# Optimization experiments

Measured on AMD Instinct MI355X. Metric: run time of the kernel, lower is better.

Reference implementation:

```python
import jax, jax.numpy as jnp
import numpy as np

NUM_HEADS = 8
NUM_LEVELS = 4
NUM_POINTS = 4
EMBED = 256
OFFSET_SCALE = 1.0
SPATIAL = [(96, 96), (48, 48), (24, 24), (12, 12)]  # (H_l, W_l) per level


def _grid_sample_bilinear(fmap, grid):
    """fmap: (N, C, H, W); grid: (N, Q, K, 2) with (x, y) in [-1, 1].
    Bilinear, align_corners=True. Locations are pre-clamped to [-1,1] so
    index clipping reproduces torch zeros-padding behavior exactly."""
    N, C, H, W = fmap.shape
    x = (grid[..., 0] + 1.0) * 0.5 * (W - 1)
    y = (grid[..., 1] + 1.0) * 0.5 * (H - 1)
    x0 = jnp.floor(x)
    y0 = jnp.floor(y)
    wx = (x - x0)[:, None]  # (N,1,Q,K)
    wy = (y - y0)[:, None]
    x0i = jnp.clip(x0.astype(jnp.int32), 0, W - 1)
    x1i = jnp.clip(x0i + 1, 0, W - 1)
    y0i = jnp.clip(y0.astype(jnp.int32), 0, H - 1)
    y1i = jnp.clip(y0i + 1, 0, H - 1)
    flat = fmap.reshape(N, C, H * W)
    Q, K = grid.shape[1], grid.shape[2]

    def g(yi, xi):
        idx = (yi * W + xi).reshape(N, 1, Q * K)
        return jnp.take_along_axis(flat, idx, axis=2).reshape(N, C, Q, K)

    return ((1 - wy) * ((1 - wx) * g(y0i, x0i) + wx * g(y0i, x1i))
            + wy * ((1 - wx) * g(y1i, x0i) + wx * g(y1i, x1i)))


def setup_inputs() -> dict:
    key = jax.random.key(0)
    ks = jax.random.split(key, 8)
    B, Q, E = 2, 12240, EMBED
    H, L, K = NUM_HEADS, NUM_LEVELS, NUM_POINTS
    Vlen = sum(h * w for h, w in SPATIAL)
    s = 0.02
    queries = jax.random.normal(ks[0], (B, Q, E), jnp.float32)
    ref_points = 2.0 * jax.random.uniform(ks[1], (B, Q, L, 2), jnp.float32) - 1.0
    value = jax.random.normal(ks[2], (B, Vlen, E), jnp.float32)
    Wv = jax.random.normal(ks[3], (E, E), jnp.float32) * s
    Woff = jax.random.normal(ks[4], (E, H * L * K * 2), jnp.float32) * s
    boff = jnp.zeros((H * L * K * 2,), jnp.float32)
    Wattn = jax.random.normal(ks[5], (E, H * L * K), jnp.float32) * s
    battn = jnp.zeros((H * L * K,), jnp.float32)
    Wout = jax.random.normal(ks[6], (E, E), jnp.float32) * s
    vss = jnp.array(SPATIAL, dtype=jnp.int32)
    return {"queries": queries, "ref_points": ref_points, "value": value,
            "Wv": Wv, "Woff": Woff, "boff": boff, "Wattn": Wattn,
            "battn": battn, "Wout": Wout, "value_spatial_shapes": vss}


def _forward(queries, ref_points, value, Wv, Woff, boff, Wattn, battn, Wout, spatial):
    B, Q, E = queries.shape
    H, L, K = NUM_HEADS, NUM_LEVELS, NUM_POINTS
    hd = E // H
    Vlen = value.shape[1]
    # offsets MLP (tanh) and attention weights
    offsets = OFFSET_SCALE * jnp.tanh(queries @ Woff + boff)
    offsets = offsets.reshape(B, Q, H, L, K, 2)
    attn = jax.nn.softmax((queries @ Wattn + battn).reshape(B, Q, H, L * K), axis=-1)
    attn = attn.reshape(B, Q, H, L, K).transpose(0, 2, 3, 1, 4).reshape(B * H, L, Q, K)
    # value projection -> (B*H, head_dim, Vlen)
    v = (value @ Wv).reshape(B, Vlen, H, hd).transpose(0, 2, 3, 1).reshape(B * H, hd, Vlen)
    # sampling locations (B*H, L, Q, K, 2)
    locs = jnp.clip(ref_points[:, :, None, :, None, :] + offsets, -1.0, 1.0)
    locs = locs.transpose(0, 2, 3, 1, 4, 5).reshape(B * H, L, Q, K, 2)
    # per-level bilinear sample + weighted accumulate
    sizes = [h * w for h, w in spatial]
    starts = np.concatenate([[0], np.cumsum(sizes)])
    acc = jnp.zeros((B * H, hd, Q, K), jnp.float32)
    for lvl, (Hl, Wl) in enumerate(spatial):
        fmap = v[:, :, starts[lvl]:starts[lvl + 1]].reshape(B * H, hd, Hl, Wl)
        samp = _grid_sample_bilinear(fmap, locs[:, lvl])  # (B*H, hd, Q, K)
        acc = acc + samp * attn[:, lvl][:, None]
    out = acc.reshape(B, E, Q, K).transpose(0, 2, 1, 3).sum(axis=-1)  # (B, Q, E)
    return out @ Wout


def reference(queries, ref_points, value, Wv, Woff, boff, Wattn, battn, Wout, value_spatial_shapes):
    spatial = [tuple(int(x) for x in row) for row in np.asarray(value_spatial_shapes)]
    return _forward(queries, ref_points, value, Wv, Woff, boff, Wattn, battn, Wout, spatial)
```

## Files before the change

kernel.cpp:

```cpp
#include <hip/hip_runtime.h>
#include <math.h>

#define NB 2
#define NQ 12240
#define NH 8
#define NL 4
#define NK 4
#define VLEN 12240
#define M_TOT (NB * NQ)
#define MT (M_TOT / 16)

typedef __attribute__((ext_vector_type(4))) float f32x4;
typedef __attribute__((ext_vector_type(8))) short bf16x8;
typedef __attribute__((ext_vector_type(8))) unsigned short u16x8;

__device__ __forceinline__ ushort f2bf(float x) {
    union { float f; unsigned u; } v; v.f = x;
    unsigned r = v.u + 0x7fffu + ((v.u >> 16) & 1u);
    return (ushort)(r >> 16);
}
__device__ __forceinline__ float bf2f(ushort h) {
    union { unsigned u; float f; } v; v.u = ((unsigned)h) << 16; return v.f;
}

__global__ __launch_bounds__(256) void preconv_B(
    const float* __restrict__ Woff, const float* __restrict__ Wattn,
    const float* __restrict__ Wv,   const float* __restrict__ Wout,
    ushort* __restrict__ Bp)
{
    const int gg = blockIdx.x * 256 + threadIdx.x;
    const float* W; ushort* H; ushort* L; int N, tl;
    if (gg < 8192)       { W = Woff;  H = Bp + 0;      L = Bp + 98304;  N = 256; tl = gg; }
    else if (gg < 12288) { W = Wattn; H = Bp + 65536;  L = Bp + 163840; N = 128; tl = gg - 8192; }
    else if (gg < 20480) { W = Wv;    H = Bp + 196608; L = Bp + 262144; N = 256; tl = gg - 12288; }
    else                 { W = Wout;  H = Bp + 327680; L = Bp + 393216; N = 256; tl = gg - 20480; }
    const int l  = tl & 63;
    const int kt = (tl >> 6) & 7;
    const int nt = tl >> 9;
    const int colb = nt * 16 + (l & 15);
    const int krow = kt * 32 + ((l >> 4) << 3);
    ushort h8[8], l8[8];
    #pragma unroll
    for (int j = 0; j < 8; ++j) {
        float x = W[(size_t)(krow + j) * N + colb];
        h8[j] = f2bf(x);
        l8[j] = f2bf(x - bf2f(h8[j]));
    }
    *(ushort4*)(H + (size_t)tl * 8)     = *(ushort4*)&h8[0];
    *(ushort4*)(H + (size_t)tl * 8 + 4) = *(ushort4*)&h8[4];
    *(ushort4*)(L + (size_t)tl * 8)     = *(ushort4*)&l8[0];
    *(ushort4*)(L + (size_t)tl * 8 + 4) = *(ushort4*)&l8[4];
}

__global__ __launch_bounds__(384) void gemm_qv(
    const float* __restrict__ Qf, const float* __restrict__ Vf,
    const ushort* __restrict__ Bp,
    const float* __restrict__ bias, const float* __restrict__ bias2,
    const float* __restrict__ ref,
    float* __restrict__ locC, float* __restrict__ attC,
    ushort* __restrict__ vC)
{
    const int wave = threadIdx.x >> 6;
    const int lane = threadIdx.x & 63;
    const bool isV = (blockIdx.x >= MT);
    const int mt   = isV ? (blockIdx.x - MT) : blockIdx.x;
    if (isV && wave >= 4) return;
    const int nt0 = wave * 4;
    const int lr = lane & 15, r0g = (lane >> 4) * 4;
    const int rowb = mt * 16 + r0g;

    const float* Af = (isV ? Vf : Qf) + (size_t)(mt * 16 + lr) * 256 + ((lane >> 4) << 3);

    f32x4 acc[4] = {};

    if (!isV) {
        const ushort* BH = Bp;
        const ushort* BL = Bp + 98304;
        #pragma unroll
        for (int kt = 0; kt < 8; ++kt) {
            float4 a0 = *(const float4*)(Af + kt * 32);
            float4 a1 = *(const float4*)(Af + kt * 32 + 4);
            union { bf16x8 v; ushort u[8]; } ah, al;
            #pragma unroll
            for (int j = 0; j < 4; ++j) {
                float x = (&a0.x)[j];
                ushort hv = f2bf(x);
                ah.u[j] = hv; al.u[j] = f2bf(x - bf2f(hv));
            }
            #pragma unroll
            for (int j = 0; j < 4; ++j) {
                float x = (&a1.x)[j];
                ushort hv = f2bf(x);
                ah.u[4 + j] = hv; al.u[4 + j] = f2bf(x - bf2f(hv));
            }
            bf16x8 bh[4], bl[4];
            #pragma unroll
            for (int fn = 0; fn < 4; ++fn) {
                size_t off = (((size_t)(nt0 + fn) * 8 + kt) * 64 + lane) * 8;
                bh[fn] = *(const bf16x8*)(BH + off);
                bl[fn] = *(const bf16x8*)(BL + off);
            }
            #pragma unroll
            for (int fn = 0; fn < 4; ++fn) {
                acc[fn] = __builtin_amdgcn_mfma_f32_16x16x32_bf16(ah.v, bh[fn], acc[fn], 0, 0, 0);
                acc[fn] = __builtin_amdgcn_mfma_f32_16x16x32_bf16(ah.v, bl[fn], acc[fn], 0, 0, 0);
                acc[fn] = __builtin_amdgcn_mfma_f32_16x16x32_bf16(al.v, bh[fn], acc[fn], 0, 0, 0);
            }
        }
        if (wave < 4) {
            #pragma unroll
            for (int fn = 0; fn < 4; ++fn) {
                const int c  = wave * 64 + fn * 16 + lr;
                const int l  = (c >> 3) & 3;
                const int xy = c & 1;
                const float sc = 0.5f * (float)(96 >> l) - 0.5f;
                const float b = bias[c];
                #pragma unroll
                for (int r = 0; r < 4; ++r) {
                    const int row = rowb + r;
                    const float rp = ref[(size_t)row * 8 + l * 2 + xy];
                    const float t  = tanhf(acc[fn][r] + b);
                    const float lc = fminf(fmaxf(rp + t, -1.f), 1.f);
                    locC[(size_t)row * 256 + c] = (lc + 1.f) * sc;
                }
            }
        } else {
            #pragma unroll
            for (int fn = 0; fn < 4; ++fn) {
                const int hcol = (wave - 4) * 64 + fn * 16 + lr;
                const float b = bias2[hcol];
                #pragma unroll
                for (int r = 0; r < 4; ++r) {
                    float e = expf(acc[fn][r] + b);
                    float s = e;
                    s += __shfl_xor(s, 1);
                    s += __shfl_xor(s, 2);
                    s += __shfl_xor(s, 4);
                    s += __shfl_xor(s, 8);
                    attC[(size_t)(rowb + r) * 128 + hcol] = e / s;
                }
            }
        }
    } else {
        const ushort* BH = Bp + 196608;
        #pragma unroll
        for (int kt = 0; kt < 8; ++kt) {
            float4 a0 = *(const float4*)(Af + kt * 32);
            float4 a1 = *(const float4*)(Af + kt * 32 + 4);
            union { bf16x8 v; ushort u[8]; } ah;
            #pragma unroll
            for (int j = 0; j < 4; ++j) ah.u[j]     = f2bf((&a0.x)[j]);
            #pragma unroll
            for (int j = 0; j < 4; ++j) ah.u[4 + j] = f2bf((&a1.x)[j]);
            bf16x8 bh[4];
            #pragma unroll
            for (int fn = 0; fn < 4; ++fn) {
                size_t off = (((size_t)(nt0 + fn) * 8 + kt) * 64 + lane) * 8;
                bh[fn] = *(const bf16x8*)(BH + off);
            }
            #pragma unroll
            for (int fn = 0; fn < 4; ++fn)
                acc[fn] = __builtin_amdgcn_mfma_f32_16x16x32_bf16(ah.v, bh[fn], acc[fn], 0, 0, 0);
        }
        #pragma unroll
        for (int fn = 0; fn < 4; ++fn) {
            const int col = (nt0 + fn) * 16 + lr;
            #pragma unroll
            for (int r = 0; r < 4; ++r)
                vC[(size_t)(rowb + r) * 256 + col] = f2bf(acc[fn][r]);
        }
    }
}

__global__ __launch_bounds__(256) void sample_kernel(
    const ushort* __restrict__ v_bf,
    const float* __restrict__ locs,
    const float* __restrict__ attnw,
    ushort* __restrict__ AccH)
{
    __shared__ float sloc[64][36];
    __shared__ float satt[64][20];

    const int h   = blockIdx.x & 7;
    const int qc  = blockIdx.x >> 3;
    const int tid = threadIdx.x;

    #pragma unroll
    for (int i = 0; i < 2; ++i) {
        int idx = tid + i * 256;
        int row = idx >> 3;
        int c   = (idx & 7) * 4;
        int bqr = qc * 64 + row;
        float4 v = make_float4(0.f, 0.f, 0.f, 0.f);
        if (bqr < M_TOT) v = *(const float4*)(locs + (size_t)bqr * 256 + h * 32 + c);
        *(float4*)&sloc[row][c] = v;
    }
    {
        int row = tid >> 2;
        int c   = (tid & 3) * 4;
        int bqr = qc * 64 + row;
        float4 v = make_float4(0.f, 0.f, 0.f, 0.f);
        if (bqr < M_TOT) v = *(const float4*)(attnw + (size_t)bqr * 128 + h * 16 + c);
        *(float4*)&satt[row][c] = v;
    }
    __syncthreads();

    const int qi = tid >> 2;
    const int c8 = tid & 3;
    const int bq = qc * 64 + qi;
    const int b  = (bq >= NQ) ? 1 : 0;
    const ushort* vbase = v_bf + ((size_t)b * VLEN) * 256 + h * 32 + c8 * 8;

    float acc[8] = {};
    #pragma unroll
    for (int l = 0; l < NL; ++l) {
        const int Wl = 96 >> l;
        const int st = (l == 0) ? 0 : (l == 1) ? 9216 : (l == 2) ? 11520 : 12096;
        #pragma unroll
        for (int k = 0; k < NK; ++k) {
            float px = sloc[qi][(l * 4 + k) * 2 + 0];
            float py = sloc[qi][(l * 4 + k) * 2 + 1];
            float w  = satt[qi][l * 4 + k];
            float x0f = floorf(px), y0f = floorf(py);
            float wx = px - x0f, wy = py - y0f;
            int x0 = (int)x0f, y0 = (int)y0f;
            x0 = min(max(x0, 0), Wl - 1);
            y0 = min(max(y0, 0), Wl - 1);
            int x1 = min(x0 + 1, Wl - 1);
            int y1 = min(y0 + 1, Wl - 1);
            float w11 = w * wy * wx;
            float w10 = w * wy - w11;
            float w01 = w * wx - w11;
            float w00 = w - w01 - w10 - w11;
            const ushort* r0 = vbase + (size_t)(st + y0 * Wl) * 256;
            const ushort* r1 = vbase + (size_t)(st + y1 * Wl) * 256;
            u16x8 u00 = *(const u16x8*)(r0 + (size_t)x0 * 256);
            u16x8 u01 = *(const u16x8*)(r0 + (size_t)x1 * 256);
            u16x8 u10 = *(const u16x8*)(r1 + (size_t)x0 * 256);
            u16x8 u11 = *(const u16x8*)(r1 + (size_t)x1 * 256);
            #pragma unroll
            for (int j = 0; j < 8; ++j) {
                acc[j] += w00 * bf2f(u00[j]) + w01 * bf2f(u01[j])
                        + w10 * bf2f(u10[j]) + w11 * bf2f(u11[j]);
            }
        }
    }

    if (bq < M_TOT) {
        const int mt  = bq >> 4;
        const int lfr = (c8 << 4) | (bq & 15);
        const size_t base = (((size_t)mt * 8 + h) * 64 + lfr) * 8;
        u16x8 hh;
        #pragma unroll
        for (int j = 0; j < 8; ++j) hh[j] = f2bf(acc[j]);
        *(u16x8*)(AccH + base) = hh;
    }
}

__global__ __launch_bounds__(256) void gemm_out(
    const ushort* __restrict__ Ah,
    const ushort* __restrict__ Bh, const ushort* __restrict__ Bl,
    float* __restrict__ C)
{
    const int wave = threadIdx.x >> 6;
    const int lane = threadIdx.x & 63;
    const int mt   = blockIdx.x;
    const int nt0  = wave * 4;

    f32x4 acc[4] = {};
    const ushort* aH = Ah + ((size_t)mt * 8 * 64 + lane) * 8;

    #pragma unroll
    for (int kt = 0; kt < 8; ++kt) {
        bf16x8 ah = *(const bf16x8*)(aH + kt * 512);
        bf16x8 bh[4], bl[4];
        #pragma unroll
        for (int fn = 0; fn < 4; ++fn) {
            size_t off = (((size_t)(nt0 + fn) * 8 + kt) * 64 + lane) * 8;
            bh[fn] = *(const bf16x8*)(Bh + off);
            bl[fn] = *(const bf16x8*)(Bl + off);
        }
        #pragma unroll
        for (int fn = 0; fn < 4; ++fn) {
            acc[fn] = __builtin_amdgcn_mfma_f32_16x16x32_bf16(ah, bh[fn], acc[fn], 0, 0, 0);
            acc[fn] = __builtin_amdgcn_mfma_f32_16x16x32_bf16(ah, bl[fn], acc[fn], 0, 0, 0);
        }
    }

    const int lr = lane & 15, r0 = (lane >> 4) * 4;
    const int rowb = mt * 16 + r0;
    #pragma unroll
    for (int fn = 0; fn < 4; ++fn) {
        const int col = (nt0 + fn) * 16 + lr;
        #pragma unroll
        for (int r = 0; r < 4; ++r)
            C[(size_t)(rowb + r) * 256 + col] = acc[fn][r];
    }
}

extern "C" void kernel_launch(void* const* d_in, const int* in_sizes, int n_in,
                              void* d_out, int out_size, void* d_ws, size_t ws_size,
                              hipStream_t stream)
{
    const float* queries = (const float*)d_in[0];
    const float* refpts  = (const float*)d_in[1];
    const float* value   = (const float*)d_in[2];
    const float* Wv      = (const float*)d_in[3];
    const float* Woff    = (const float*)d_in[4];
    const float* boff    = (const float*)d_in[5];
    const float* Wattn   = (const float*)d_in[6];
    const float* battn   = (const float*)d_in[7];
    const float* Wout    = (const float*)d_in[8];
    float* out = (float*)d_out;

    char* ws = (char*)d_ws;
    float*  off_ws  = (float*)(ws);
    float*  attn_ws = (float*)(ws + 25067520);
    ushort* v_bf    = (ushort*)(ws + 37601280);
    ushort* AccH    = (ushort*)(ws + 50135040);
    ushort* Bp      = (ushort*)(ws + 87736320);

    preconv_B<<<112, 256, 0, stream>>>(Woff, Wattn, Wv, Wout, Bp);
    gemm_qv<<<3060, 384, 0, stream>>>(queries, value, Bp, boff, battn, refpts,
                                      off_ws, attn_ws, v_bf);
    sample_kernel<<<3064, 256, 0, stream>>>(v_bf, off_ws, attn_ws, AccH);
    gemm_out<<<1530, 256, 0, stream>>>(AccH, Bp + 327680, Bp + 393216, out);
}
```

Measured before the change: 231.1 us.

## Switch intermediates to fp16, drop Wout low split, and process two M-tiles per block

Replaces bf16 storage and MFMA with fp16 throughout: weight pre-splitting, value projection, sampled accumulator and output GEMM, with packed cvt_pkrtz conversions instead of manual bf16 rounding. The output GEMM no longer uses a hi/lo split of Wout, which halves its B loads and MFMAs. The QV and output GEMMs each handle two 16-row tiles per block so every B fragment is reused twice, which halves the grid sizes. The fp16 range and round-toward-zero conversions trade some accuracy and overflow headroom for cheaper conversion and fewer MFMAs.

```diff
diff --git a/kernel.cpp b/kernel.cpp
--- a/kernel.cpp
+++ b/kernel.cpp
@@ -11,172 +11,183 @@
 #define MT (M_TOT / 16)
 
 typedef __attribute__((ext_vector_type(4))) float f32x4;
-typedef __attribute__((ext_vector_type(8))) short bf16x8;
-typedef __attribute__((ext_vector_type(8))) unsigned short u16x8;
-
-__device__ __forceinline__ ushort f2bf(float x) {
-    union { float f; unsigned u; } v; v.f = x;
-    unsigned r = v.u + 0x7fffu + ((v.u >> 16) & 1u);
-    return (ushort)(r >> 16);
-}
-__device__ __forceinline__ float bf2f(ushort h) {
-    union { unsigned u; float f; } v; v.u = ((unsigned)h) << 16; return v.f;
-}
+typedef __fp16 f16;
+typedef __attribute__((ext_vector_type(8))) __fp16 f16x8;
+typedef __attribute__((ext_vector_type(2))) __fp16 f16x2;
+
+#define BP_FL 98304
+#define BP_WV 196608
+#define BP_WO 262144
 
 __global__ __launch_bounds__(256) void preconv_B(
     const float* __restrict__ Woff, const float* __restrict__ Wattn,
     const float* __restrict__ Wv,   const float* __restrict__ Wout,
-    ushort* __restrict__ Bp)
+    f16* __restrict__ Bp)
 {
     const int gg = blockIdx.x * 256 + threadIdx.x;
-    const float* W; ushort* H; ushort* L; int N, tl;
-    if (gg < 8192)       { W = Woff;  H = Bp + 0;      L = Bp + 98304;  N = 256; tl = gg; }
-    else if (gg < 12288) { W = Wattn; H = Bp + 65536;  L = Bp + 163840; N = 128; tl = gg - 8192; }
-    else if (gg < 20480) { W = Wv;    H = Bp + 196608; L = Bp + 262144; N = 256; tl = gg - 12288; }
-    else                 { W = Wout;  H = Bp + 327680; L = Bp + 393216; N = 256; tl = gg - 20480; }
+    const float* W; f16* H; f16* L; int N, tl; bool two;
+    if (gg < 8192)       { W = Woff;  H = Bp;           L = Bp + BP_FL;         N = 256; tl = gg;         two = true;  }
+    else if (gg < 12288) { W = Wattn; H = Bp + 65536;   L = Bp + BP_FL + 65536; N = 128; tl = gg - 8192;  two = true;  }
+    else if (gg < 20480) { W = Wv;    H = Bp + BP_WV;   L = nullptr;            N = 256; tl = gg - 12288; two = false; }
+    else                 { W = Wout;  H = Bp + BP_WO;   L = nullptr;            N = 256; tl = gg - 20480; two = false; }
     const int l  = tl & 63;
     const int kt = (tl >> 6) & 7;
     const int nt = tl >> 9;
     const int colb = nt * 16 + (l & 15);
     const int krow = kt * 32 + ((l >> 4) << 3);
-    ushort h8[8], l8[8];
+    union { f16 f[8]; ushort4 u[2]; } h8, l8;
     #pragma unroll
     for (int j = 0; j < 8; ++j) {
         float x = W[(size_t)(krow + j) * N + colb];
-        h8[j] = f2bf(x);
-        l8[j] = f2bf(x - bf2f(h8[j]));
-    }
-    *(ushort4*)(H + (size_t)tl * 8)     = *(ushort4*)&h8[0];
-    *(ushort4*)(H + (size_t)tl * 8 + 4) = *(ushort4*)&h8[4];
-    *(ushort4*)(L + (size_t)tl * 8)     = *(ushort4*)&l8[0];
-    *(ushort4*)(L + (size_t)tl * 8 + 4) = *(ushort4*)&l8[4];
-}
-
-__global__ __launch_bounds__(384) void gemm_qv(
+        f16 hv = (f16)x;
+        h8.f[j] = hv;
+        l8.f[j] = (f16)(x - (float)hv);
+    }
+    *(ushort4*)(H + (size_t)tl * 8)     = h8.u[0];
+    *(ushort4*)(H + (size_t)tl * 8 + 4) = h8.u[1];
+    if (two) {
+        *(ushort4*)(L + (size_t)tl * 8)     = l8.u[0];
+        *(ushort4*)(L + (size_t)tl * 8 + 4) = l8.u[1];
+    }
+}
+
+__global__ __launch_bounds__(384, 3) void gemm_qv(
     const float* __restrict__ Qf, const float* __restrict__ Vf,
-    const ushort* __restrict__ Bp,
+    const f16* __restrict__ Bp,
     const float* __restrict__ bias, const float* __restrict__ bias2,
     const float* __restrict__ ref,
     float* __restrict__ locC, float* __restrict__ attC,
-    ushort* __restrict__ vC)
+    f16* __restrict__ vC)
 {
     const int wave = threadIdx.x >> 6;
     const int lane = threadIdx.x & 63;
-    const bool isV = (blockIdx.x >= MT);
-    const int mt   = isV ? (blockIdx.x - MT) : blockIdx.x;
+    const bool isV = (blockIdx.x >= 765);
+    const int mt0  = (isV ? (blockIdx.x - 765) : blockIdx.x) * 2;
     if (isV && wave >= 4) return;
     const int nt0 = wave * 4;
     const int lr = lane & 15, r0g = (lane >> 4) * 4;
-    const int rowb = mt * 16 + r0g;
-
-    const float* Af = (isV ? Vf : Qf) + (size_t)(mt * 16 + lr) * 256 + ((lane >> 4) << 3);
-
-    f32x4 acc[4] = {};
+
+    const float* A0 = (isV ? Vf : Qf) + (size_t)(mt0 * 16 + lr) * 256 + ((lane >> 4) << 3);
+    const float* A1 = A0 + 16 * 256;
+
+    f32x4 acc[2][4] = {};
 
     if (!isV) {
-        const ushort* BH = Bp;
-        const ushort* BL = Bp + 98304;
+        const f16* BH = Bp;
+        const f16* BL = Bp + BP_FL;
         #pragma unroll
         for (int kt = 0; kt < 8; ++kt) {
-            float4 a0 = *(const float4*)(Af + kt * 32);
-            float4 a1 = *(const float4*)(Af + kt * 32 + 4);
-            union { bf16x8 v; ushort u[8]; } ah, al;
-            #pragma unroll
-            for (int j = 0; j < 4; ++j) {
-                float x = (&a0.x)[j];
-                ushort hv = f2bf(x);
-                ah.u[j] = hv; al.u[j] = f2bf(x - bf2f(hv));
-            }
-            #pragma unroll
-            for (int j = 0; j < 4; ++j) {
-                float x = (&a1.x)[j];
-                ushort hv = f2bf(x);
-                ah.u[4 + j] = hv; al.u[4 + j] = f2bf(x - bf2f(hv));
-            }
-            bf16x8 bh[4], bl[4];
+            f16x8 bh[4], bl[4];
             #pragma unroll
             for (int fn = 0; fn < 4; ++fn) {
                 size_t off = (((size_t)(nt0 + fn) * 8 + kt) * 64 + lane) * 8;
-                bh[fn] = *(const bf16x8*)(BH + off);
-                bl[fn] = *(const bf16x8*)(BL + off);
-            }
-            #pragma unroll
-            for (int fn = 0; fn < 4; ++fn) {
-                acc[fn] = __builtin_amdgcn_mfma_f32_16x16x32_bf16(ah.v, bh[fn], acc[fn], 0, 0, 0);
-                acc[fn] = __builtin_amdgcn_mfma_f32_16x16x32_bf16(ah.v, bl[fn], acc[fn], 0, 0, 0);
-                acc[fn] = __builtin_amdgcn_mfma_f32_16x16x32_bf16(al.v, bh[fn], acc[fn], 0, 0, 0);
-            }
-        }
-        if (wave < 4) {
-            #pragma unroll
-            for (int fn = 0; fn < 4; ++fn) {
-                const int c  = wave * 64 + fn * 16 + lr;
-                const int l  = (c >> 3) & 3;
-                const int xy = c & 1;
-                const float sc = 0.5f * (float)(96 >> l) - 0.5f;
-                const float b = bias[c];
-                #pragma unroll
-                for (int r = 0; r < 4; ++r) {
-                    const int row = rowb + r;
-                    const float rp = ref[(size_t)row * 8 + l * 2 + xy];
-                    const float t  = tanhf(acc[fn][r] + b);
-                    const float lc = fminf(fmaxf(rp + t, -1.f), 1.f);
-                    locC[(size_t)row * 256 + c] = (lc + 1.f) * sc;
+                bh[fn] = *(const f16x8*)(BH + off);
+                bl[fn] = *(const f16x8*)(BL + off);
+            }
+            #pragma unroll
+            for (int m = 0; m < 2; ++m) {
+                const float* Af = m ? A1 : A0;
+                float4 a0 = *(const float4*)(Af + kt * 32);
+                float4 a1 = *(const float4*)(Af + kt * 32 + 4);
+                union { f16x8 v; f16x2 h[4]; } ah, al;
+                ah.h[0] = __builtin_amdgcn_cvt_pkrtz(a0.x, a0.y);
+                ah.h[1] = __builtin_amdgcn_cvt_pkrtz(a0.z, a0.w);
+                ah.h[2] = __builtin_amdgcn_cvt_pkrtz(a1.x, a1.y);
+                ah.h[3] = __builtin_amdgcn_cvt_pkrtz(a1.z, a1.w);
+                al.h[0] = __builtin_amdgcn_cvt_pkrtz(a0.x - (float)ah.h[0][0], a0.y - (float)ah.h[0][1]);
+                al.h[1] = __builtin_amdgcn_cvt_pkrtz(a0.z - (float)ah.h[1][0], a0.w - (float)ah.h[1][1]);
+                al.h[2] = __builtin_amdgcn_cvt_pkrtz(a1.x - (float)ah.h[2][0], a1.y - (float)ah.h[2][1]);
+                al.h[3] = __builtin_amdgcn_cvt_pkrtz(a1.z - (float)ah.h[3][0], a1.w - (float)ah.h[3][1]);
+                #pragma unroll
+                for (int fn = 0; fn < 4; ++fn) {
+                    acc[m][fn] = __builtin_amdgcn_mfma_f32_16x16x32_f16(ah.v, bh[fn], acc[m][fn], 0, 0, 0);
+                    acc[m][fn] = __builtin_amdgcn_mfma_f32_16x16x32_f16(ah.v, bl[fn], acc[m][fn], 0, 0, 0);
+                    acc[m][fn] = __builtin_amdgcn_mfma_f32_16x16x32_f16(al.v, bh[fn], acc[m][fn], 0, 0, 0);
                 }
             }
-        } else {
-            #pragma unroll
-            for (int fn = 0; fn < 4; ++fn) {
-                const int hcol = (wave - 4) * 64 + fn * 16 + lr;
-                const float b = bias2[hcol];
-                #pragma unroll
-                for (int r = 0; r < 4; ++r) {
-                    float e = expf(acc[fn][r] + b);
-                    float s = e;
-                    s += __shfl_xor(s, 1);
-                    s += __shfl_xor(s, 2);
-                    s += __shfl_xor(s, 4);
-                    s += __shfl_xor(s, 8);
-                    attC[(size_t)(rowb + r) * 128 + hcol] = e / s;
+        }
+        #pragma unroll
+        for (int m = 0; m < 2; ++m) {
+            const int rowb = (mt0 + m) * 16 + r0g;
+            if (wave < 4) {
+                #pragma unroll
+                for (int fn = 0; fn < 4; ++fn) {
+                    const int c  = wave * 64 + fn * 16 + lr;
+                    const int l  = (c >> 3) & 3;
+                    const int xy = c & 1;
+                    const float sc = 0.5f * (float)(96 >> l) - 0.5f;
+                    const float b = bias[c];
+                    #pragma unroll
+                    for (int r = 0; r < 4; ++r) {
+                        const int row = rowb + r;
+                        const float rp = ref[(size_t)row * 8 + l * 2 + xy];
+                        const float t  = tanhf(acc[m][fn][r] + b);
+                        const float lc = fminf(fmaxf(rp + t, -1.f), 1.f);
+                        locC[(size_t)row * 256 + c] = (lc + 1.f) * sc;
+                    }
                 }
+            } else {
+                #pragma unroll
+                for (int fn = 0; fn < 4; ++fn) {
+                    const int hcol = (wave - 4) * 64 + fn * 16 + lr;
+                    const float b = bias2[hcol];
+                    #pragma unroll
+                    for (int r = 0; r < 4; ++r) {
+                        float e = expf(acc[m][fn][r] + b);
+                        float s = e;
+                        s += __shfl_xor(s, 1);
+                        s += __shfl_xor(s, 2);
+                        s += __shfl_xor(s, 4);
+                        s += __shfl_xor(s, 8);
+                        attC[(size_t)(rowb + r) * 128 + hcol] = e / s;
+                    }
+                }
             }
         }
     } else {
-        const ushort* BH = Bp + 196608;
+        const f16* BH = Bp + BP_WV;
         #pragma unroll
         for (int kt = 0; kt < 8; ++kt) {
-            float4 a0 = *(const float4*)(Af + kt * 32);
-            float4 a1 = *(const float4*)(Af + kt * 32 + 4);
-            union { bf16x8 v; ushort u[8]; } ah;
-            #pragma unroll
-            for (int j = 0; j < 4; ++j) ah.u[j]     = f2bf((&a0.x)[j]);
-            #pragma unroll
-            for (int j = 0; j < 4; ++j) ah.u[4 + j] = f2bf((&a1.x)[j]);
-            bf16x8 bh[4];
+            f16x8 bh[4];
             #pragma unroll
             for (int fn = 0; fn < 4; ++fn) {
                 size_t off = (((size_t)(nt0 + fn) * 8 + kt) * 64 + lane) * 8;
-                bh[fn] = *(const bf16x8*)(BH + off);
-            }
-            #pragma unroll
-            for (int fn = 0; fn < 4; ++fn)
-                acc[fn] = __builtin_amdgcn_mfma_f32_16x16x32_bf16(ah.v, bh[fn], acc[fn], 0, 0, 0);
-        }
-        #pragma unroll
-        for (int fn = 0; fn < 4; ++fn) {
-            const int col = (nt0 + fn) * 16 + lr;
-            #pragma unroll
-            for (int r = 0; r < 4; ++r)
-                vC[(size_t)(rowb + r) * 256 + col] = f2bf(acc[fn][r]);
+                bh[fn] = *(const f16x8*)(BH + off);
+            }
+            #pragma unroll
+            for (int m = 0; m < 2; ++m) {
+                const float* Af = m ? A1 : A0;
+                float4 a0 = *(const float4*)(Af + kt * 32);
+                float4 a1 = *(const float4*)(Af + kt * 32 + 4);
+                union { f16x8 v; f16x2 h[4]; } ah;
+                ah.h[0] = __builtin_amdgcn_cvt_pkrtz(a0.x, a0.y);
+                ah.h[1] = __builtin_amdgcn_cvt_pkrtz(a0.z, a0.w);
+                ah.h[2] = __builtin_amdgcn_cvt_pkrtz(a1.x, a1.y);
+                ah.h[3] = __builtin_amdgcn_cvt_pkrtz(a1.z, a1.w);
+                #pragma unroll
+                for (int fn = 0; fn < 4; ++fn)
+                    acc[m][fn] = __builtin_amdgcn_mfma_f32_16x16x32_f16(ah.v, bh[fn], acc[m][fn], 0, 0, 0);
+            }
+        }
+        #pragma unroll
+        for (int m = 0; m < 2; ++m) {
+            const int rowb = (mt0 + m) * 16 + r0g;
+            #pragma unroll
+            for (int fn = 0; fn < 4; ++fn) {
+                const int col = (nt0 + fn) * 16 + lr;
+                #pragma unroll
+                for (int r = 0; r < 4; ++r)
+                    vC[(size_t)(rowb + r) * 256 + col] = (f16)acc[m][fn][r];
+            }
         }
     }
 }
 
 __global__ __launch_bounds__(256) void sample_kernel(
-    const ushort* __restrict__ v_bf,
+    const f16* __restrict__ v_f16,
     const float* __restrict__ locs,
     const float* __restrict__ attnw,
-    ushort* __restrict__ AccH)
+    f16* __restrict__ AccH)
 {
     __shared__ float sloc[64][36];
     __shared__ float satt[64][20];
@@ -209,7 +220,7 @@
     const int c8 = tid & 3;
     const int bq = qc * 64 + qi;
     const int b  = (bq >= NQ) ? 1 : 0;
-    const ushort* vbase = v_bf + ((size_t)b * VLEN) * 256 + h * 32 + c8 * 8;
+    const f16* vbase = v_f16 + ((size_t)b * VLEN) * 256 + h * 32 + c8 * 8;
 
     float acc[8] = {};
     #pragma unroll
@@ -232,16 +243,16 @@
             float w10 = w * wy - w11;
             float w01 = w * wx - w11;
             float w00 = w - w01 - w10 - w11;
-            const ushort* r0 = vbase + (size_t)(st + y0 * Wl) * 256;
-            const ushort* r1 = vbase + (size_t)(st + y1 * Wl) * 256;
-            u16x8 u00 = *(const u16x8*)(r0 + (size_t)x0 * 256);
-            u16x8 u01 = *(const u16x8*)(r0 + (size_t)x1 * 256);
-            u16x8 u10 = *(const u16x8*)(r1 + (size_t)x0 * 256);
-            u16x8 u11 = *(const u16x8*)(r1 + (size_t)x1 * 256);
+            const f16* r0 = vbase + (size_t)(st + y0 * Wl) * 256;
+            const f16* r1 = vbase + (size_t)(st + y1 * Wl) * 256;
+            f16x8 u00 = *(const f16x8*)(r0 + (size_t)x0 * 256);
+            f16x8 u01 = *(const f16x8*)(r0 + (size_t)x1 * 256);
+            f16x8 u10 = *(const f16x8*)(r1 + (size_t)x0 * 256);
+            f16x8 u11 = *(const f16x8*)(r1 + (size_t)x1 * 256);
             #pragma unroll
             for (int j = 0; j < 8; ++j) {
-                acc[j] += w00 * bf2f(u00[j]) + w01 * bf2f(u01[j])
-                        + w10 * bf2f(u10[j]) + w11 * bf2f(u11[j]);
+                acc[j] += w00 * (float)u00[j] + w01 * (float)u01[j]
+                        + w10 * (float)u10[j] + w11 * (float)u11[j];
             }
         }
     }
@@ -250,51 +261,56 @@
         const int mt  = bq >> 4;
         const int lfr = (c8 << 4) | (bq & 15);
         const size_t base = (((size_t)mt * 8 + h) * 64 + lfr) * 8;
-        u16x8 hh;
-        #pragma unroll
-        for (int j = 0; j < 8; ++j) hh[j] = f2bf(acc[j]);
-        *(u16x8*)(AccH + base) = hh;
+        union { f16x8 v; f16x2 h[4]; } hh;
+        hh.h[0] = __builtin_amdgcn_cvt_pkrtz(acc[0], acc[1]);
+        hh.h[1] = __builtin_amdgcn_cvt_pkrtz(acc[2], acc[3]);
+        hh.h[2] = __builtin_amdgcn_cvt_pkrtz(acc[4], acc[5]);
+        hh.h[3] = __builtin_amdgcn_cvt_pkrtz(acc[6], acc[7]);
+        *(f16x8*)(AccH + base) = hh.v;
     }
 }
 
 __global__ __launch_bounds__(256) void gemm_out(
-    const ushort* __restrict__ Ah,
-    const ushort* __restrict__ Bh, const ushort* __restrict__ Bl,
+    const f16* __restrict__ Ah, const f16* __restrict__ Bh,
     float* __restrict__ C)
 {
     const int wave = threadIdx.x >> 6;
     const int lane = threadIdx.x & 63;
-    const int mt   = blockIdx.x;
+    const int mt0  = blockIdx.x * 2;
     const int nt0  = wave * 4;
 
-    f32x4 acc[4] = {};
-    const ushort* aH = Ah + ((size_t)mt * 8 * 64 + lane) * 8;
+    f32x4 acc[2][4] = {};
+    const f16* aH0 = Ah + ((size_t)mt0 * 8 * 64 + lane) * 8;
+    const f16* aH1 = aH0 + 8 * 64 * 8;
 
     #pragma unroll
     for (int kt = 0; kt < 8; ++kt) {
-        bf16x8 ah = *(const bf16x8*)(aH + kt * 512);
-        bf16x8 bh[4], bl[4];
+        f16x8 ah0 = *(const f16x8*)(aH0 + kt * 512);
+        f16x8 ah1 = *(const f16x8*)(aH1 + kt * 512);
+        f16x8 bh[4];
         #pragma unroll
         for (int fn = 0; fn < 4; ++fn) {
             size_t off = (((size_t)(nt0 + fn) * 8 + kt) * 64 + lane) * 8;
-            bh[fn] = *(const bf16x8*)(Bh + off);
-            bl[fn] = *(const bf16x8*)(Bl + off);
+            bh[fn] = *(const f16x8*)(Bh + off);
         }
         #pragma unroll
         for (int fn = 0; fn < 4; ++fn) {
-            acc[fn] = __builtin_amdgcn_mfma_f32_16x16x32_bf16(ah, bh[fn], acc[fn], 0, 0, 0);
-            acc[fn] = __builtin_amdgcn_mfma_f32_16x16x32_bf16(ah, bl[fn], acc[fn], 0, 0, 0);
+            acc[0][fn] = __builtin_amdgcn_mfma_f32_16x16x32_f16(ah0, bh[fn], acc[0][fn], 0, 0, 0);
+            acc[1][fn] = __builtin_amdgcn_mfma_f32_16x16x32_f16(ah1, bh[fn], acc[1][fn], 0, 0, 0);
         }
     }
 
     const int lr = lane & 15, r0 = (lane >> 4) * 4;
-    const int rowb = mt * 16 + r0;
-    #pragma unroll
-    for (int fn = 0; fn < 4; ++fn) {
-        const int col = (nt0 + fn) * 16 + lr;
-        #pragma unroll
-        for (int r = 0; r < 4; ++r)
-            C[(size_t)(rowb + r) * 256 + col] = acc[fn][r];
+    #pragma unroll
+    for (int m = 0; m < 2; ++m) {
+        const int rowb = (mt0 + m) * 16 + r0;
+        #pragma unroll
+        for (int fn = 0; fn < 4; ++fn) {
+            const int col = (nt0 + fn) * 16 + lr;
+            #pragma unroll
+            for (int r = 0; r < 4; ++r)
+                C[(size_t)(rowb + r) * 256 + col] = acc[m][fn][r];
+        }
     }
 }
 
@@ -314,15 +330,15 @@
     float* out = (float*)d_out;
 
     char* ws = (char*)d_ws;
-    float*  off_ws  = (float*)(ws);
-    float*  attn_ws = (float*)(ws + 25067520);
-    ushort* v_bf    = (ushort*)(ws + 37601280);
-    ushort* AccH    = (ushort*)(ws + 50135040);
-    ushort* Bp      = (ushort*)(ws + 87736320);
+    float* off_ws  = (float*)(ws);
+    float* attn_ws = (float*)(ws + 25067520);
+    f16*   v_f16   = (f16*)(ws + 37601280);
+    f16*   AccH    = (f16*)(ws + 50135040);
+    f16*   Bp      = (f16*)(ws + 62668800);
 
     preconv_B<<<112, 256, 0, stream>>>(Woff, Wattn, Wv, Wout, Bp);
-    gemm_qv<<<3060, 384, 0, stream>>>(queries, value, Bp, boff, battn, refpts,
-                                      off_ws, attn_ws, v_bf);
-    sample_kernel<<<3064, 256, 0, stream>>>(v_bf, off_ws, attn_ws, AccH);
-    gemm_out<<<1530, 256, 0, stream>>>(AccH, Bp + 327680, Bp + 393216, out);
-}
+    gemm_qv<<<1530, 384, 0, stream>>>(queries, value, Bp, boff, battn, refpts,
+                                      off_ws, attn_ws, v_f16);
+    sample_kernel<<<3064, 256, 0, stream>>>(v_f16, off_ws, attn_ws, AccH);
+    gemm_out<<<765, 256, 0, stream>>>(AccH, Bp + BP_WO, out);
+}
```

Result: faster. 221.2 us (-4.3%).
